# Performance work log

Hardware: AMD Instinct MI355X
Metric: run time of the kernel (lower is better)

Reference implementation:

```python
import jax, jax.numpy as jnp
import numpy as np

BN_EPS = 1e-5


def setup_inputs() -> dict:
    key = jax.random.key(0)
    ks = jax.random.split(key, 13)
    B, C, H, W = 32, 256, 96, 48
    return {
        "x": jax.random.normal(ks[0], (B, C, H, W), dtype=jnp.float32),
        "g_w": jax.random.normal(ks[1], (C,), dtype=jnp.float32),
        "g_b": jax.random.normal(ks[2], (1,), dtype=jnp.float32),
        "theta_w": jax.random.normal(ks[3], (C,), dtype=jnp.float32),
        "theta_b": jax.random.normal(ks[4], (1,), dtype=jnp.float32),
        "phi_w": jax.random.normal(ks[5], (C,), dtype=jnp.float32),
        "phi_b": jax.random.normal(ks[6], (1,), dtype=jnp.float32),
        "W_w": jax.random.normal(ks[7], (C,), dtype=jnp.float32),
        "W_b": jax.random.normal(ks[8], (C,), dtype=jnp.float32),
        "bn_gamma": jax.random.normal(ks[9], (C,), dtype=jnp.float32),
        "bn_beta": jax.random.normal(ks[10], (C,), dtype=jnp.float32),
        "bn_mean": jax.random.normal(ks[11], (C,), dtype=jnp.float32),
        "bn_var": jax.random.uniform(ks[12], (C,), dtype=jnp.float32),
    }


def reference(x, g_w, g_b, theta_w, theta_b, phi_w, phi_b, W_w, W_b,
              bn_gamma, bn_beta, bn_mean, bn_var):
    # x: (B, C, H, W); inter_channels == 1 so all 1x1 convs are channel dots.
    B, C, H, Wd = x.shape
    N = H * Wd
    xf = x.reshape(B, C, N)  # (B, C, N)

    g = jnp.einsum("c,bcn->bn", g_w, xf) + g_b          # (B, N)
    theta = jnp.einsum("c,bcn->bn", theta_w, xf) + theta_b
    phi = jnp.einsum("c,bcn->bn", phi_w, xf) + phi_b

    # f_div_C @ g_x == theta * (phi . g) / N  (rank-1 contraction, exact by associativity)
    s = jnp.sum(phi * g, axis=1) / N                     # (B,)
    y = theta * s[:, None]                               # (B, N), inter_channels dim is 1

    # W: 1x1 conv 1->C, then BatchNorm (inference form), then residual add.
    Wy = y[:, None, :] * W_w[None, :, None] + W_b[None, :, None]  # (B, C, N)
    inv_std = bn_gamma / jnp.sqrt(bn_var + BN_EPS)                 # (C,)
    bn = (Wy - bn_mean[None, :, None]) * inv_std[None, :, None] + bn_beta[None, :, None]

    z = bn.reshape(B, C, H, Wd) + x
    return z
```

## Files before the change

### kernel.cpp

```cpp
#include <hip/hip_runtime.h>

constexpr int Bn = 32;
constexpr int Cn = 256;
constexpr int Hn = 96;
constexpr int Wn = 48;
constexpr int Nn = Hn * Wn;
constexpr int N4 = Nn / 4;
constexpr float BN_EPS = 1e-5f;

__global__ __launch_bounds__(512) void pass1_kernel(
    const float* __restrict__ x,
    const float* __restrict__ g_w, const float* __restrict__ g_b,
    const float* __restrict__ theta_w, const float* __restrict__ theta_b,
    const float* __restrict__ phi_w, const float* __restrict__ phi_b,
    float* __restrict__ theta_out,
    float* __restrict__ s_out)
{
    __shared__ float wg[Cn], wt[Cn], wp[Cn];
    __shared__ float4 red[3][8][64];

    const int tid  = threadIdx.x;
    const int lane = tid & 63;
    const int wave = tid >> 6;

    if (tid < Cn) {
        wg[tid] = g_w[tid];
        wt[tid] = theta_w[tid];
        wp[tid] = phi_w[tid];
    }
    __syncthreads();

    const int bx = blockIdx.x;
    const int b  = bx / 18;
    const int n4 = (bx % 18) * 64 + lane;

    const float4* xb = reinterpret_cast<const float4*>(x)
                     + (size_t)b * (size_t)(Cn * N4) + n4;

    float4 ag = {0.f, 0.f, 0.f, 0.f};
    float4 at = {0.f, 0.f, 0.f, 0.f};
    float4 ap = {0.f, 0.f, 0.f, 0.f};

    const int c0 = wave * 32;
    #pragma unroll 8
    for (int cc = 0; cc < 32; ++cc) {
        const int c = c0 + cc;
        const float4 xv = xb[(size_t)c * N4];
        const float cg = wg[c], ct = wt[c], cp = wp[c];
        ag.x = fmaf(cg, xv.x, ag.x);
        ag.y = fmaf(cg, xv.y, ag.y);
        ag.z = fmaf(cg, xv.z, ag.z);
        ag.w = fmaf(cg, xv.w, ag.w);
        at.x = fmaf(ct, xv.x, at.x);
        at.y = fmaf(ct, xv.y, at.y);
        at.z = fmaf(ct, xv.z, at.z);
        at.w = fmaf(ct, xv.w, at.w);
        ap.x = fmaf(cp, xv.x, ap.x);
        ap.y = fmaf(cp, xv.y, ap.y);
        ap.z = fmaf(cp, xv.z, ap.z);
        ap.w = fmaf(cp, xv.w, ap.w);
    }

    red[0][wave][lane] = ag;
    red[1][wave][lane] = at;
    red[2][wave][lane] = ap;
    __syncthreads();

    if (wave == 0) {
        float4 sg = red[0][0][lane];
        float4 st = red[1][0][lane];
        float4 sp = red[2][0][lane];
        #pragma unroll
        for (int w = 1; w < 8; ++w) {
            const float4 rg = red[0][w][lane];
            const float4 rt = red[1][w][lane];
            const float4 rp = red[2][w][lane];
            sg.x += rg.x; sg.y += rg.y; sg.z += rg.z; sg.w += rg.w;
            st.x += rt.x; st.y += rt.y; st.z += rt.z; st.w += rt.w;
            sp.x += rp.x; sp.y += rp.y; sp.z += rp.z; sp.w += rp.w;
        }

        const float gb = g_b[0], tb = theta_b[0], pb = phi_b[0];

        float4 th;
        th.x = st.x + tb; th.y = st.y + tb; th.z = st.z + tb; th.w = st.w + tb;
        reinterpret_cast<float4*>(theta_out)[(size_t)b * N4 + n4] = th;

        float p = (sg.x + gb) * (sp.x + pb)
                + (sg.y + gb) * (sp.y + pb)
                + (sg.z + gb) * (sp.z + pb)
                + (sg.w + gb) * (sp.w + pb);

        #pragma unroll
        for (int off = 32; off > 0; off >>= 1)
            p += __shfl_down(p, off);

        if (lane == 0)
            atomicAdd(&s_out[b], p);
    }
}

__global__ __launch_bounds__(256) void pass2_kernel(
    const float* __restrict__ x,
    const float* __restrict__ theta_buf,
    const float* __restrict__ s_buf,
    const float* __restrict__ W_w, const float* __restrict__ W_b,
    const float* __restrict__ bn_gamma, const float* __restrict__ bn_beta,
    const float* __restrict__ bn_mean, const float* __restrict__ bn_var,
    float* __restrict__ out)
{
    constexpr int total4 = Bn * Cn * N4;
    const int stride = gridDim.x * blockDim.x;
    const float invN = 1.0f / (float)Nn;

    for (int idx = blockIdx.x * blockDim.x + threadIdx.x;
         idx < total4; idx += stride) {
        const int b   = idx / (Cn * N4);
        const int rem = idx - b * (Cn * N4);
        const int c   = rem / N4;
        const int n4  = rem - c * N4;

        const float inv_std = bn_gamma[c] * rsqrtf(bn_var[c] + BN_EPS);
        const float a = W_w[c] * inv_std;
        const float d = fmaf(W_b[c] - bn_mean[c], inv_std, bn_beta[c]);
        const float sb = s_buf[b] * invN;

        const float4 th = reinterpret_cast<const float4*>(theta_buf)[b * N4 + n4];
        const float4 xv = reinterpret_cast<const float4*>(x)[idx];

        float4 o;
        o.x = fmaf(th.x * sb, a, d) + xv.x;
        o.y = fmaf(th.y * sb, a, d) + xv.y;
        o.z = fmaf(th.z * sb, a, d) + xv.z;
        o.w = fmaf(th.w * sb, a, d) + xv.w;

        reinterpret_cast<float4*>(out)[idx] = o;
    }
}

extern "C" void kernel_launch(void* const* d_in, const int* in_sizes, int n_in,
                              void* d_out, int out_size, void* d_ws, size_t ws_size,
                              hipStream_t stream) {
    const float* x        = (const float*)d_in[0];
    const float* g_w      = (const float*)d_in[1];
    const float* g_b      = (const float*)d_in[2];
    const float* theta_w  = (const float*)d_in[3];
    const float* theta_b  = (const float*)d_in[4];
    const float* phi_w    = (const float*)d_in[5];
    const float* phi_b    = (const float*)d_in[6];
    const float* W_w      = (const float*)d_in[7];
    const float* W_b      = (const float*)d_in[8];
    const float* bn_gamma = (const float*)d_in[9];
    const float* bn_beta  = (const float*)d_in[10];
    const float* bn_mean  = (const float*)d_in[11];
    const float* bn_var   = (const float*)d_in[12];

    float* out = (float*)d_out;

    float* theta_buf = (float*)d_ws;
    float* s_buf     = (float*)((char*)d_ws + (size_t)Bn * Nn * sizeof(float));

    hipMemsetAsync(s_buf, 0, Bn * sizeof(float), stream);

    pass1_kernel<<<Bn * 18, 512, 0, stream>>>(
        x, g_w, g_b, theta_w, theta_b, phi_w, phi_b, theta_buf, s_buf);

    pass2_kernel<<<2048, 256, 0, stream>>>(
        x, theta_buf, s_buf, W_w, W_b, bn_gamma, bn_beta, bn_mean, bn_var, out);
}
```

Baseline: 83.07 us.

## Replace atomic reduction with per-tile partials; restructure pass2 with nontemporal stores

Pass1 now writes per-tile partial dot products instead of atomically accumulating, which removes the memset launch and the atomics. Pass2 reduces the 18 partials per batch at block start, and each thread loads theta once and reuses it across 32 channels in a 2D grid (36 x 32 blocks). Output is written with nontemporal stores so the streamed result does not pollute cache. The trade-offs are fewer blocks (1152) with more work per thread, and strided per-channel parameter loads.

```diff
diff --git a/kernel.cpp b/kernel.cpp
--- a/kernel.cpp
+++ b/kernel.cpp
@@ -6,7 +6,10 @@
 constexpr int Wn = 48;
 constexpr int Nn = Hn * Wn;
 constexpr int N4 = Nn / 4;
+constexpr int TILES = 18;
 constexpr float BN_EPS = 1e-5f;
+
+typedef float floatx4 __attribute__((ext_vector_type(4)));
 
 __global__ __launch_bounds__(512) void pass1_kernel(
     const float* __restrict__ x,
@@ -14,7 +17,7 @@
     const float* __restrict__ theta_w, const float* __restrict__ theta_b,
     const float* __restrict__ phi_w, const float* __restrict__ phi_b,
     float* __restrict__ theta_out,
-    float* __restrict__ s_out)
+    float* __restrict__ part_out)
 {
     __shared__ float wg[Cn], wt[Cn], wp[Cn];
     __shared__ float4 red[3][8][64];
@@ -30,9 +33,10 @@
     }
     __syncthreads();
 
-    const int bx = blockIdx.x;
-    const int b  = bx / 18;
-    const int n4 = (bx % 18) * 64 + lane;
+    const int bx   = blockIdx.x;
+    const int b    = bx / TILES;
+    const int tile = bx % TILES;
+    const int n4   = tile * 64 + lane;
 
     const float4* xb = reinterpret_cast<const float4*>(x)
                      + (size_t)b * (size_t)(Cn * N4) + n4;
@@ -96,45 +100,62 @@
             p += __shfl_down(p, off);
 
         if (lane == 0)
-            atomicAdd(&s_out[b], p);
+            part_out[b * TILES + tile] = p;
     }
 }
 
 __global__ __launch_bounds__(256) void pass2_kernel(
     const float* __restrict__ x,
     const float* __restrict__ theta_buf,
-    const float* __restrict__ s_buf,
+    const float* __restrict__ part_buf,
     const float* __restrict__ W_w, const float* __restrict__ W_b,
     const float* __restrict__ bn_gamma, const float* __restrict__ bn_beta,
     const float* __restrict__ bn_mean, const float* __restrict__ bn_var,
     float* __restrict__ out)
 {
-    constexpr int total4 = Bn * Cn * N4;
-    const int stride = gridDim.x * blockDim.x;
-    const float invN = 1.0f / (float)Nn;
+    __shared__ float s_sh;
+    const int tid = threadIdx.x;
+    const int b   = blockIdx.y;
 
-    for (int idx = blockIdx.x * blockDim.x + threadIdx.x;
-         idx < total4; idx += stride) {
-        const int b   = idx / (Cn * N4);
-        const int rem = idx - b * (Cn * N4);
-        const int c   = rem / N4;
-        const int n4  = rem - c * N4;
+    if (tid < 64) {
+        float p = (tid < TILES) ? part_buf[b * TILES + tid] : 0.0f;
+        #pragma unroll
+        for (int off = 16; off > 0; off >>= 1)
+            p += __shfl_down(p, off);
+        if (tid == 0) s_sh = p * (1.0f / (float)Nn);
+    }
+    __syncthreads();
+    const float sb = s_sh;
 
+    const int tg  = blockIdx.x * 256 + tid;
+    const int c00 = tg / N4;
+    const int n4  = tg - c00 * N4;
+
+    const float4* xb  = reinterpret_cast<const float4*>(x)
+                      + (size_t)b * (size_t)(Cn * N4);
+    floatx4*      ob  = reinterpret_cast<floatx4*>(out)
+                      + (size_t)b * (size_t)(Cn * N4);
+    const float4  th  = reinterpret_cast<const float4*>(theta_buf)[(size_t)b * N4 + n4];
+    const float   tsx = th.x * sb, tsy = th.y * sb,
+                  tsz = th.z * sb, tsw = th.w * sb;
+
+    #pragma unroll
+    for (int it = 0; it < Cn / 8; ++it) {
+        const int c = c00 + it * 8;
         const float inv_std = bn_gamma[c] * rsqrtf(bn_var[c] + BN_EPS);
         const float a = W_w[c] * inv_std;
         const float d = fmaf(W_b[c] - bn_mean[c], inv_std, bn_beta[c]);
-        const float sb = s_buf[b] * invN;
 
-        const float4 th = reinterpret_cast<const float4*>(theta_buf)[b * N4 + n4];
-        const float4 xv = reinterpret_cast<const float4*>(x)[idx];
+        const size_t idx = (size_t)c * N4 + n4;
+        const float4 xv = xb[idx];
 
-        float4 o;
-        o.x = fmaf(th.x * sb, a, d) + xv.x;
-        o.y = fmaf(th.y * sb, a, d) + xv.y;
-        o.z = fmaf(th.z * sb, a, d) + xv.z;
-        o.w = fmaf(th.w * sb, a, d) + xv.w;
+        floatx4 o;
+        o.x = fmaf(tsx, a, d) + xv.x;
+        o.y = fmaf(tsy, a, d) + xv.y;
+        o.z = fmaf(tsz, a, d) + xv.z;
+        o.w = fmaf(tsw, a, d) + xv.w;
 
-        reinterpret_cast<float4*>(out)[idx] = o;
+        __builtin_nontemporal_store(o, &ob[idx]);
     }
 }
 
@@ -158,13 +179,12 @@
     float* out = (float*)d_out;
 
     float* theta_buf = (float*)d_ws;
-    float* s_buf     = (float*)((char*)d_ws + (size_t)Bn * Nn * sizeof(float));
+    float* part_buf  = (float*)((char*)d_ws + (size_t)Bn * Nn * sizeof(float));
 
-    hipMemsetAsync(s_buf, 0, Bn * sizeof(float), stream);
+    pass1_kernel<<<Bn * TILES, 512, 0, stream>>>(
+        x, g_w, g_b, theta_w, theta_b, phi_w, phi_b, theta_buf, part_buf);
 
-    pass1_kernel<<<Bn * 18, 512, 0, stream>>>(
-        x, g_w, g_b, theta_w, theta_b, phi_w, phi_b, theta_buf, s_buf);
-
-    pass2_kernel<<<2048, 256, 0, stream>>>(
-        x, theta_buf, s_buf, W_w, W_b, bn_gamma, bn_beta, bn_mean, bn_var, out);
+    dim3 g2(36, Bn);
+    pass2_kernel<<<g2, 256, 0, stream>>>(
+        x, theta_buf, part_buf, W_w, W_b, bn_gamma, bn_beta, bn_mean, bn_var, out);
 }
```

Result: faster. 77.07 us (-7.2%).
